# Performance work log

Hardware: AMD Instinct MI355X
Metric: run time of the kernel (lower is better)

## Reference

```python
import jax, jax.numpy as jnp
import numpy as np

N = 30000   # nodes
E = 300000  # edges
B = 64      # graphs
H = 4       # heads
C = 64      # channels per head
HC = H * C  # 256


def setup_inputs() -> dict:
    key = jax.random.key(0)
    ks = jax.random.split(key, 32)

    def rn(k, shape):
        scale = 1.0 / np.sqrt(shape[0])
        return (jax.random.normal(k, shape) * scale).astype(jnp.float32)

    inp = {}
    inp["x"] = jax.random.normal(ks[0], (N, 13), dtype=jnp.float32)
    inp["edge_index"] = jax.random.randint(ks[1], (2, E), 0, N, dtype=jnp.int64)
    inp["edge_attr"] = jax.random.normal(ks[2], (E, 51), dtype=jnp.float32)
    inp["batch"] = jnp.sort(jax.random.randint(ks[3], (N,), 0, B, dtype=jnp.int64))
    # init node MLP: Linear(13 -> 128) (plain_last => no act/norm)
    inp["W0"] = rn(ks[4], (13, 128)); inp["b0"] = jnp.zeros((128,), jnp.float32)
    # GATv2 layer 1: in 128 -> H=4, C=64
    inp["Wl1"] = rn(ks[5], (128, HC)); inp["bl1"] = jnp.zeros((HC,), jnp.float32)
    inp["Wr1"] = rn(ks[6], (128, HC)); inp["br1"] = jnp.zeros((HC,), jnp.float32)
    inp["We1"] = rn(ks[7], (51, HC))
    inp["att1"] = rn(ks[8], (H, C))
    inp["bias1"] = jnp.zeros((HC,), jnp.float32)
    # GATv2 layer 2: in 256 -> H=4, C=64
    inp["Wl2"] = rn(ks[9], (HC, HC)); inp["bl2"] = jnp.zeros((HC,), jnp.float32)
    inp["Wr2"] = rn(ks[10], (HC, HC)); inp["br2"] = jnp.zeros((HC,), jnp.float32)
    inp["We2"] = rn(ks[11], (51, HC))
    inp["att2"] = rn(ks[12], (H, C))
    inp["bias2"] = jnp.zeros((HC,), jnp.float32)
    # attention pooling MLP: Linear(256 -> 256) (plain_last)
    inp["Wp"] = rn(ks[13], (HC, HC)); inp["bp"] = jnp.zeros((HC,), jnp.float32)
    # out MLP: Linear(256->256)+BN+ReLU, Linear(256->2001)
    inp["Wo1"] = rn(ks[14], (HC, 256)); inp["bo1"] = jnp.zeros((256,), jnp.float32)
    inp["gamma"] = jnp.ones((256,), jnp.float32); inp["beta"] = jnp.zeros((256,), jnp.float32)
    inp["Wo2"] = rn(ks[15], (256, 2001)); inp["bo2"] = jnp.zeros((2001,), jnp.float32)
    return inp


def _gatv2(x, src, dst, ea, Wl, bl, Wr, br, We, att, bias):
    n = x.shape[0]
    xl = (x @ Wl + bl).reshape(n, H, C)   # source transform (also message content)
    xr = (x @ Wr + br).reshape(n, H, C)   # target transform
    ee = (ea @ We).reshape(-1, H, C)      # edge embedding, no bias
    z = jax.nn.leaky_relu(xl[src] + xr[dst] + ee, negative_slope=0.2)  # [E,H,C]
    logit = jnp.einsum('ehc,hc->eh', z, att)                           # [E,H]
    m = jax.ops.segment_max(logit, dst, num_segments=n)                # [N,H]
    w = jnp.exp(logit - m[dst])
    den = jax.ops.segment_sum(w, dst, num_segments=n)
    alpha = w / (den[dst] + 1e-16)                                     # segment softmax
    out = jax.ops.segment_sum(xl[src] * alpha[:, :, None], dst, num_segments=n)
    return out.reshape(n, HC) + bias


def _forward(x, edge_index, edge_attr, batch, W0, b0, Wl1, bl1, Wr1, br1, We1, att1, bias1,
             Wl2, bl2, Wr2, br2, We2, att2, bias2, Wp, bp, Wo1, bo1, gamma, beta, Wo2, bo2):
    src, dst = edge_index[0], edge_index[1]
    h = x @ W0 + b0
    h = _gatv2(h, src, dst, edge_attr, Wl1, bl1, Wr1, br1, We1, att1, bias1)
    h = _gatv2(h, src, dst, edge_attr, Wl2, bl2, Wr2, br2, We2, att2, bias2)
    # softmax attention pooling over nodes of each graph (per feature column)
    a = h @ Wp + bp                                       # [N,HC]
    am = jax.ops.segment_max(a, batch, num_segments=B)
    aw = jnp.exp(a - am[batch])
    ad = jax.ops.segment_sum(aw, batch, num_segments=B)
    attw = aw / (ad[batch] + 1e-16)
    g = jax.ops.segment_sum(h * attw, batch, num_segments=B)  # [B,HC]
    # out MLP: Linear + BatchNorm(train stats) + ReLU + Linear, then leaky_relu
    y = g @ Wo1 + bo1
    mu = jnp.mean(y, axis=0)
    var = jnp.var(y, axis=0)
    y = (y - mu) / jnp.sqrt(var + 1e-5) * gamma + beta
    y = jax.nn.relu(y)
    y = y @ Wo2 + bo2
    return jax.nn.leaky_relu(y, negative_slope=0.01)


def reference(x, edge_index, edge_attr, batch, W0, b0, Wl1, bl1, Wr1, br1, We1, att1, bias1,
              Wl2, bl2, Wr2, br2, We2, att2, bias2, Wp, bp, Wo1, bo1, gamma, beta, Wo2, bo2):
    return _forward(x, edge_index, edge_attr, batch, W0, b0, Wl1, bl1, Wr1, br1, We1, att1, bias1,
                    Wl2, bl2, Wr2, br2, We2, att2, bias2, Wp, bp, Wo1, bo1, gamma, beta, Wo2, bo2)
```

## Files before the change

kernel.cpp:

```cpp
#include <hip/hip_runtime.h>
#include <hip/hip_bf16.h>

#define NN 30000
#define EE 300000
#define BB 64
#define HH 4
#define CC 64
#define HC 256

typedef __attribute__((ext_vector_type(8))) short short8;
typedef __attribute__((ext_vector_type(4))) float floatx4;

__device__ __forceinline__ float b2f(short x) {
    return __uint_as_float(((unsigned)(unsigned short)x) << 16);
}
__device__ __forceinline__ unsigned short f2b(float f) {
    __hip_bfloat16 h = __float2bfloat16(f);
    return *(unsigned short*)&h;
}

#define GLD16(gp, lp) __builtin_amdgcn_global_load_lds( \
    (const __attribute__((address_space(1))) void*)(gp), \
    (__attribute__((address_space(3))) void*)(lp), 16, 0, 0)

#define ROT2(x) ((((x) << 2) | ((x) >> 3)) & 31)
#define EESWZ(chunk, row) (ROT2(chunk) ^ (((row) >> 2) & 3) ^ (((row) & 1) << 2))

template<int CT>
__global__ __launch_bounds__(256) void mfma_gemm(
    const ushort* __restrict__ A, const ushort* __restrict__ Bt,
    const float* __restrict__ bias, float* __restrict__ outF,
    __hip_bfloat16* __restrict__ outB, int M, int Nc, int K) {
    __shared__ __align__(16) ushort lA[64 * 32];
    __shared__ __align__(16) ushort lB[CT * 64 * 32];
    const int tid = threadIdx.x, lane = tid & 63, wv = tid >> 6;
    const int row0 = blockIdx.x * 64, col0 = blockIdx.y * (CT * 64);

    floatx4 acc[4][CT];
#pragma unroll
    for (int r = 0; r < 4; r++)
#pragma unroll
        for (int c = 0; c < CT; c++) acc[r][c] = (floatx4){0.f, 0.f, 0.f, 0.f};

    const int arow = tid >> 2;
    const int sl   = (tid & 3) ^ ((tid >> 3) & 3);
    const ushort* ga = A + (size_t)(row0 + arow) * K + sl * 8;
    const int m16 = lane & 15, q = lane >> 4;

    for (int k0 = 0; k0 < K; k0 += 32) {
        __syncthreads();
        GLD16(ga + k0, &lA[tid * 8]);
#pragma unroll
        for (int j = 0; j < CT; j++) {
            const ushort* gb = Bt + (size_t)(col0 + j * 64 + arow) * K + k0 + sl * 8;
            GLD16(gb, &lB[j * 2048 + tid * 8]);
        }
        __syncthreads();
        short8 aF[4], bF[CT];
#pragma unroll
        for (int r = 0; r < 4; r++) {
            int rr = r * 16 + m16;
            aF[r] = *(const short8*)&lA[rr * 32 + ((q ^ ((rr >> 1) & 3)) << 3)];
        }
#pragma unroll
        for (int c = 0; c < CT; c++) {
            int nr = (wv * CT + c) * 16 + m16;
            bF[c] = *(const short8*)&lB[nr * 32 + ((q ^ ((nr >> 1) & 3)) << 3)];
        }
#pragma unroll
        for (int r = 0; r < 4; r++)
#pragma unroll
            for (int c = 0; c < CT; c++)
                acc[r][c] = __builtin_amdgcn_mfma_f32_16x16x32_bf16(aF[r], bF[c], acc[r][c], 0, 0, 0);
    }

#pragma unroll
    for (int c = 0; c < CT; c++) {
        int col = col0 + (wv * CT + c) * 16 + m16;
        float bv = bias ? bias[col] : 0.f;
#pragma unroll
        for (int r = 0; r < 4; r++)
#pragma unroll
            for (int j = 0; j < 4; j++) {
                int row = row0 + r * 16 + q * 4 + j;
                if (row < M) {
                    float v = acc[r][c][j] + bv;
                    if (outB) outB[(size_t)row * Nc + col] = __float2bfloat16(v);
                    else      outF[(size_t)row * Nc + col] = v;
                }
            }
    }
}

__global__ void permute_ea_frag(const float* __restrict__ ea,
                                const int* __restrict__ eidx,
                                ushort* __restrict__ ea_frag) {
    const int t = threadIdx.x, tile = blockIdx.x;
    const int r  = t >> 6;
    const int ch = (t >> 3) & 7;
    const int m0 = (t * 2) & 15;
    ushort* outp = ea_frag + (size_t)tile * 4096 + t * 16;
#pragma unroll
    for (int half = 0; half < 2; half++) {
        int row = r * 16 + m0 + half;
        int gi = tile * 64 + row;
        int e = (gi < EE) ? eidx[gi] : -1;
        short8 v8;
#pragma unroll
        for (int j = 0; j < 8; j++) {
            int k = ch * 8 + j;
            float v = (e >= 0 && k < 51) ? ea[(size_t)e * 51 + k] : 0.f;
            v8[j] = (short)f2b(v);
        }
        *(short8*)(outp + half * 8) = v8;
    }
}

__global__ void pack_we_frag(const float* __restrict__ WeA,
                             const float* __restrict__ WeB,
                             ushort* __restrict__ WfA, ushort* __restrict__ WfB) {
    const float* We = blockIdx.y ? WeB : WeA;
    ushort* Wf = blockIdx.y ? WfB : WfA;
    int o = blockIdx.x * 256 + threadIdx.x;
    int j = o & 7, m16 = (o >> 3) & 15, ch = (o >> 7) & 7, nt = o >> 10;
    int n = nt * 16 + m16, k = ch * 8 + j;
    float v = (k < 51) ? We[k * 256 + n] : 0.f;
    Wf[o] = f2b(v);
}

__global__ __launch_bounds__(256, 4) void edge_fused(
    const ushort* __restrict__ ea_frag, const ushort* __restrict__ Wfrag,
    const float* __restrict__ att,
    const int* __restrict__ src_csr, const int* __restrict__ dst_csr,
    const ushort* __restrict__ xlr, float* __restrict__ logitp) {
    __shared__ __align__(16) ushort eeS[64 * 256];
    __shared__ float satt[256];
    const int tid = threadIdx.x, lane = tid & 63, wv = tid >> 6;
    const int i0 = blockIdx.x * 64;
    satt[tid] = att[tid];
    const int m16 = lane & 15, q = lane >> 4;

    floatx4 acc[4][4];
#pragma unroll
    for (int r = 0; r < 4; r++)
#pragma unroll
        for (int c = 0; c < 4; c++) acc[r][c] = (floatx4){0.f, 0.f, 0.f, 0.f};

    const ushort* af = ea_frag + (size_t)blockIdx.x * 4096;
#pragma unroll
    for (int k0 = 0; k0 < 2; k0++) {
        short8 aF[4], bF[4];
#pragma unroll
        for (int r = 0; r < 4; r++)
            aF[r] = *(const short8*)&af[((r * 8 + k0 * 4 + q) * 16 + m16) * 8];
#pragma unroll
        for (int c = 0; c < 4; c++)
            bF[c] = *(const short8*)&Wfrag[(((wv * 4 + c) * 8 + k0 * 4 + q) * 16 + m16) * 8];
#pragma unroll
        for (int r = 0; r < 4; r++)
#pragma unroll
            for (int c = 0; c < 4; c++)
                acc[r][c] = __builtin_amdgcn_mfma_f32_16x16x32_bf16(aF[r], bF[c], acc[r][c], 0, 0, 0);
    }

#pragma unroll
    for (int r = 0; r < 4; r++)
#pragma unroll
        for (int cc = 0; cc < 4; cc++)
#pragma unroll
            for (int j = 0; j < 4; j++) {
                int row = r * 16 + q * 4 + j;
                int col = (wv * 4 + cc) * 16 + m16;
                int chunk = col >> 3;
                int P = EESWZ(chunk, row);
                eeS[row * 256 + (P << 3) + (col & 7)] = f2b(acc[r][cc][j]);
            }
    __syncthreads();

    const int el = tid >> 2, h = tid & 3;
    const int i = i0 + el;
    if (i < EE) {
        int src = src_csr[i], dstn = dst_csr[i];
        const ushort* xlp = xlr + (size_t)src * 512 + h * 64;
        const ushort* xrp = xlr + (size_t)dstn * 512 + 256 + h * 64;
        float s = 0.f;
#pragma unroll
        for (int c = 0; c < 8; c++) {
            short8 xlv = *(const short8*)(xlp + c * 8);
            short8 xrv = *(const short8*)(xrp + c * 8);
            int chunk = h * 8 + c;
            int P = EESWZ(chunk, el);
            short8 eev = *(const short8*)&eeS[el * 256 + (P << 3)];
#pragma unroll
            for (int j = 0; j < 8; j++) {
                float v = b2f(xlv[j]) + b2f(xrv[j]) + b2f(eev[j]);
                v = v > 0.f ? v : 0.2f * v;
                s += v * satt[h * 64 + c * 8 + j];
            }
        }
        logitp[(size_t)i * 4 + h] = s;
    }
}

__global__ void pack_x(const float* __restrict__ x, __hip_bfloat16* __restrict__ d,
                       int* __restrict__ deg) {
    int i = blockIdx.x * 256 + threadIdx.x;
    if (i < NN) deg[i] = 0;
    if (i >= NN * 32) return;
    int n = i >> 5, k = i & 31;
    d[i] = __float2bfloat16(k < 13 ? x[n * 13 + k] : 0.f);
}
struct PackJob { const float* W; __hip_bfloat16* dst; int K, Nc, Kpad, rowoff; };
struct PackJobs { PackJob j[6]; };
__global__ void pack_all(PackJobs jobs) {
    PackJob jb = jobs.j[blockIdx.y];
    int tot = jb.Nc * jb.Kpad;
    for (int i = blockIdx.x * 256 + threadIdx.x; i < tot; i += gridDim.x * 256) {
        int n = i / jb.Kpad, k = i - n * jb.Kpad;
        float v = (k < jb.K) ? jb.W[k * jb.Nc + n] : 0.f;
        jb.dst[(size_t)(jb.rowoff + n) * jb.Kpad + k] = __float2bfloat16(v);
    }
}
__global__ void cat2(const float* __restrict__ a, const float* __restrict__ b,
                     float* __restrict__ o) {
    int i = blockIdx.x * 256 + threadIdx.x;
    if (i < 512) o[i] = i < 256 ? a[i] : b[i - 256];
}

__global__ void hist_deg(const int* __restrict__ ei, int* __restrict__ deg) {
    int e = blockIdx.x * 256 + threadIdx.x;
    if (e < EE) atomicAdd(&deg[ei[EE + e]], 1);
}
__global__ void scan1(const int* __restrict__ deg, int* __restrict__ partial,
                      int* __restrict__ bsum) {
    __shared__ int sh[256];
    int t = threadIdx.x, i = blockIdx.x * 256 + t;
    int v = (i < NN) ? deg[i] : 0;
    sh[t] = v; __syncthreads();
    for (int off = 1; off < 256; off <<= 1) {
        int x = (t >= off) ? sh[t - off] : 0;
        __syncthreads();
        sh[t] += x;
        __syncthreads();
    }
    if (i < NN) partial[i] = sh[t] - v;
    if (t == 255) bsum[blockIdx.x] = sh[255];
}
__global__ void scan2(int* __restrict__ bsum, int nb) {
    __shared__ int sh[256];
    int t = threadIdx.x;
    int v = (t < nb) ? bsum[t] : 0;
    sh[t] = v; __syncthreads();
    for (int off = 1; off < 256; off <<= 1) {
        int x = (t >= off) ? sh[t - off] : 0;
        __syncthreads();
        sh[t] += x;
        __syncthreads();
    }
    if (t < nb) bsum[t] = sh[t] - v;
}
__global__ void scan3(const int* __restrict__ partial, const int* __restrict__ bsum,
                      int* __restrict__ start, int* __restrict__ cursor) {
    int i = blockIdx.x * 256 + threadIdx.x;
    if (i < NN) { start[i] = partial[i] + bsum[i >> 8]; cursor[i] = 0; }
    else if (i == NN) start[NN] = EE;
}
__global__ void scatter_e(const int* __restrict__ ei, int* __restrict__ cursor,
                          const int* __restrict__ start, int* __restrict__ eidx,
                          int* __restrict__ src_csr, int* __restrict__ dst_csr) {
    int e = blockIdx.x * 256 + threadIdx.x;
    if (e >= EE) return;
    int s = ei[e];
    int d = ei[EE + e];
    int p = atomicAdd(&cursor[d], 1);
    int pos = start[d] + p;
    eidx[pos] = e;
    src_csr[pos] = s;
    dst_csr[pos] = d;
}

__global__ __launch_bounds__(256) void aggregate_csr(
    const ushort* __restrict__ xlr, const float* __restrict__ logitp,
    const int* __restrict__ src_csr, const int* __restrict__ start,
    const float* __restrict__ bias, ushort* __restrict__ outb) {
    const int lane = threadIdx.x & 63, wv = threadIdx.x >> 6;
    const int dst = blockIdx.x * 4 + wv;
    if (dst >= NN) return;
    const int s0 = start[dst];
    const int deg = start[dst + 1] - s0;
    const int h = lane >> 4;

    float m[4] = {-3.4e38f, -3.4e38f, -3.4e38f, -3.4e38f};
    float lg[4] = {0.f, 0.f, 0.f, 0.f};
    int mysrc = 0;
    if (lane < deg) {
        mysrc = src_csr[s0 + lane];
        float4 l4 = ((const float4*)logitp)[s0 + lane];
        lg[0] = l4.x; lg[1] = l4.y; lg[2] = l4.z; lg[3] = l4.w;
        m[0] = l4.x; m[1] = l4.y; m[2] = l4.z; m[3] = l4.w;
    }
    for (int i = 64 + lane; i < deg; i += 64) {
        float4 l4 = ((const float4*)logitp)[s0 + i];
        m[0] = fmaxf(m[0], l4.x); m[1] = fmaxf(m[1], l4.y);
        m[2] = fmaxf(m[2], l4.z); m[3] = fmaxf(m[3], l4.w);
    }
#pragma unroll
    for (int off = 32; off; off >>= 1)
#pragma unroll
        for (int k = 0; k < 4; k++) m[k] = fmaxf(m[k], __shfl_xor(m[k], off));

    float w[4], d[4];
#pragma unroll
    for (int k = 0; k < 4; k++) {
        w[k] = (lane < deg) ? __expf(lg[k] - m[k]) : 0.f;
        d[k] = w[k];
    }
    for (int i = 64 + lane; i < deg; i += 64) {
        float4 l4 = ((const float4*)logitp)[s0 + i];
        d[0] += __expf(l4.x - m[0]); d[1] += __expf(l4.y - m[1]);
        d[2] += __expf(l4.z - m[2]); d[3] += __expf(l4.w - m[3]);
    }
#pragma unroll
    for (int off = 32; off; off >>= 1)
#pragma unroll
        for (int k = 0; k < 4; k++) d[k] += __shfl_xor(d[k], off);
    const float dh = 1.f / (((h == 0) ? d[0] : (h == 1) ? d[1] : (h == 2) ? d[2] : d[3]) + 1e-16f);
    const float mh = (h == 0) ? m[0] : (h == 1) ? m[1] : (h == 2) ? m[2] : m[3];

    float4 b4 = ((const float4*)bias)[lane];
    float a0 = b4.x, a1 = b4.y, a2 = b4.z, a3 = b4.w;

    const int dcap = deg < 64 ? deg : 64;
    const ushort* xbase = xlr + (size_t)lane * 4;
    int i = 0;
    for (; i + 4 <= dcap; i += 4) {
        int sv[4]; float aw[4];
#pragma unroll
        for (int u = 0; u < 4; u++) {
            sv[u] = __shfl(mysrc, i + u);
            float s0v = __shfl(w[0], i + u), s1v = __shfl(w[1], i + u);
            float s2v = __shfl(w[2], i + u), s3v = __shfl(w[3], i + u);
            aw[u] = ((h == 0) ? s0v : (h == 1) ? s1v : (h == 2) ? s2v : s3v) * dh;
        }
        ushort4 xv[4];
#pragma unroll
        for (int u = 0; u < 4; u++)
            xv[u] = *(const ushort4*)(xbase + (size_t)sv[u] * 512);
#pragma unroll
        for (int u = 0; u < 4; u++) {
            a0 += b2f(xv[u].x) * aw[u]; a1 += b2f(xv[u].y) * aw[u];
            a2 += b2f(xv[u].z) * aw[u]; a3 += b2f(xv[u].w) * aw[u];
        }
    }
    for (; i < dcap; i++) {
        int srcv = __shfl(mysrc, i);
        float s0v = __shfl(w[0], i), s1v = __shfl(w[1], i);
        float s2v = __shfl(w[2], i), s3v = __shfl(w[3], i);
        float aw = ((h == 0) ? s0v : (h == 1) ? s1v : (h == 2) ? s2v : s3v) * dh;
        ushort4 xv = *(const ushort4*)(xbase + (size_t)srcv * 512);
        a0 += b2f(xv.x) * aw; a1 += b2f(xv.y) * aw;
        a2 += b2f(xv.z) * aw; a3 += b2f(xv.w) * aw;
    }
    for (int ii = 64; ii < deg; ii++) {
        int srcv = src_csr[s0 + ii];
        float4 l4 = ((const float4*)logitp)[s0 + ii];
        float lh = (h == 0) ? l4.x : (h == 1) ? l4.y : (h == 2) ? l4.z : l4.w;
        float aw = __expf(lh - mh) * dh;
        ushort4 xv = *(const ushort4*)(xbase + (size_t)srcv * 512);
        a0 += b2f(xv.x) * aw; a1 += b2f(xv.y) * aw;
        a2 += b2f(xv.z) * aw; a3 += b2f(xv.w) * aw;
    }
    ushort4 ov;
    ov.x = f2b(a0); ov.y = f2b(a1); ov.z = f2b(a2); ov.w = f2b(a3);
    *(ushort4*)(outb + (size_t)dst * 256 + lane * 4) = ov;
}

__device__ __forceinline__ unsigned fmap(float f) {
    unsigned u = __float_as_uint(f);
    return (u & 0x80000000u) ? ~u : (u | 0x80000000u);
}
__device__ __forceinline__ float funmap(unsigned u) {
    return (u & 0x80000000u) ? __uint_as_float(u & 0x7FFFFFFFu)
                             : __uint_as_float(~u);
}

__global__ void pool_max(const float* __restrict__ a, const int* __restrict__ batch,
                         unsigned* __restrict__ am, float* __restrict__ den,
                         float* __restrict__ num) {
    const int c = threadIdx.x;
    if (blockIdx.x < BB) {
        den[blockIdx.x * HC + c] = 0.f;
        num[blockIdx.x * HC + c] = 0.f;
    }
    const int n0 = blockIdx.x * 64;
    int curb = batch[n0];
    float m = -3.4e38f;
    const int nend = min(n0 + 64, NN);
    for (int n = n0; n < nend; n++) {
        int b = batch[n];
        float v = a[(size_t)n * HC + c];
        if (b != curb) { atomicMax(&am[curb * HC + c], fmap(m)); curb = b; m = v; }
        else           { m = fmaxf(m, v); }
    }
    atomicMax(&am[curb * HC + c], fmap(m));
}
__global__ void pool_sums(const float* __restrict__ a, const __hip_bfloat16* __restrict__ h2,
                          const int* __restrict__ batch, const unsigned* __restrict__ am,
                          float* __restrict__ den, float* __restrict__ num) {
    const int c = threadIdx.x;
    const int n0 = blockIdx.x * 64;
    int curb = batch[n0];
    float sd = 0.f, sn = 0.f;
    float mcur = funmap(am[curb * HC + c]);
    const int nend = min(n0 + 64, NN);
    for (int n = n0; n < nend; n++) {
        int b = batch[n];
        if (b != curb) {
            atomicAdd(&den[curb * HC + c], sd);
            atomicAdd(&num[curb * HC + c], sn);
            curb = b; sd = 0.f; sn = 0.f; mcur = funmap(am[b * HC + c]);
        }
        float w = __expf(a[(size_t)n * HC + c] - mcur);
        sd += w;
        sn += __bfloat162float(h2[(size_t)n * HC + c]) * w;
    }
    atomicAdd(&den[curb * HC + c], sd);
    atomicAdd(&num[curb * HC + c], sn);
}

__global__ void mlp_lin1(const float* __restrict__ num, const float* __restrict__ den,
                         const float* __restrict__ Wo1, const float* __restrict__ bo1,
                         float* __restrict__ y) {
    __shared__ float gsh[HC];
    const int c = threadIdx.x;
    const int r = blockIdx.x;
    gsh[c] = num[r * HC + c] / (den[r * HC + c] + 1e-16f);
    __syncthreads();
    float acc = bo1[c];
#pragma unroll 4
    for (int k = 0; k < HC; k++) acc = fmaf(gsh[k], Wo1[k * HC + c], acc);
    y[r * HC + c] = acc;
}
__global__ void bn_relu(float* __restrict__ y, const float* __restrict__ gamma,
                        const float* __restrict__ beta) {
    const int c = threadIdx.x;
    float s = 0.f, sq = 0.f;
    for (int r = 0; r < BB; r++) { float v = y[r * HC + c]; s += v; sq += v * v; }
    float mu  = s * (1.f / BB);
    float var = sq * (1.f / BB) - mu * mu;
    float inv = rsqrtf(var + 1e-5f) * gamma[c];
    float bt  = beta[c];
    for (int r = 0; r < BB; r++) {
        float v = (y[r * HC + c] - mu) * inv + bt;
        y[r * HC + c] = v > 0.f ? v : 0.f;
    }
}
__global__ void mlp_lin2(const float* __restrict__ y, const float* __restrict__ Wo2,
                         const float* __restrict__ bo2, float* __restrict__ out) {
    const int j = blockIdx.x * 256 + threadIdx.x;
    const int r = blockIdx.y;
    if (j >= 2001) return;
    float acc = bo2[j];
#pragma unroll 4
    for (int k = 0; k < HC; k++) acc = fmaf(y[r * HC + k], Wo2[k * 2001 + j], acc);
    out[r * 2001 + j] = acc > 0.f ? acc : 0.01f * acc;
}

extern "C" void kernel_launch(void* const* d_in, const int* in_sizes, int n_in,
                              void* d_out, int out_size, void* d_ws, size_t ws_size,
                              hipStream_t stream) {
    const float* x     = (const float*)d_in[0];
    const int*   ei    = (const int*)d_in[1];
    const float* ea    = (const float*)d_in[2];
    const int*   batch = (const int*)d_in[3];
    const float* W0 = (const float*)d_in[4];  const float* b0 = (const float*)d_in[5];
    const float* Wl1 = (const float*)d_in[6]; const float* bl1 = (const float*)d_in[7];
    const float* Wr1 = (const float*)d_in[8]; const float* br1 = (const float*)d_in[9];
    const float* We1 = (const float*)d_in[10]; const float* att1 = (const float*)d_in[11];
    const float* bias1 = (const float*)d_in[12];
    const float* Wl2 = (const float*)d_in[13]; const float* bl2 = (const float*)d_in[14];
    const float* Wr2 = (const float*)d_in[15]; const float* br2 = (const float*)d_in[16];
    const float* We2 = (const float*)d_in[17]; const float* att2 = (const float*)d_in[18];
    const float* bias2 = (const float*)d_in[19];
    const float* Wp = (const float*)d_in[20]; const float* bp = (const float*)d_in[21];
    const float* Wo1 = (const float*)d_in[22]; const float* bo1 = (const float*)d_in[23];
    const float* gamma = (const float*)d_in[24]; const float* beta = (const float*)d_in[25];
    const float* Wo2 = (const float*)d_in[26]; const float* bo2 = (const float*)d_in[27];
    float* out = (float*)d_out;

    char* p = (char*)d_ws;
    auto alloc = [&](size_t bytes) { char* r = p; p += (bytes + 255) & ~(size_t)255; return r; };
    const int MP = 30016;
    const int ET = 4688;
    __hip_bfloat16* xpad  = (__hip_bfloat16*)alloc((size_t)MP * 32 * 2);
    __hip_bfloat16* W0t   = (__hip_bfloat16*)alloc(128 * 32 * 2);
    __hip_bfloat16* W1t   = (__hip_bfloat16*)alloc(512 * 128 * 2);
    __hip_bfloat16* W2t   = (__hip_bfloat16*)alloc(512 * 256 * 2);
    __hip_bfloat16* Wpt   = (__hip_bfloat16*)alloc(256 * 256 * 2);
    ushort* Wef1 = (ushort*)alloc(256 * 64 * 2);
    ushort* Wef2 = (ushort*)alloc(256 * 64 * 2);
    float* bcat1 = (float*)alloc(512 * 4);
    float* bcat2 = (float*)alloc(512 * 4);
    __hip_bfloat16* h0b  = (__hip_bfloat16*)alloc((size_t)MP * 128 * 2);
    __hip_bfloat16* xlrb = (__hip_bfloat16*)alloc((size_t)MP * 512 * 2);
    __hip_bfloat16* h1b  = (__hip_bfloat16*)alloc((size_t)MP * 256 * 2);
    __hip_bfloat16* h2b  = (__hip_bfloat16*)alloc((size_t)MP * 256 * 2);
    ushort* ea_frag = (ushort*)alloc((size_t)ET * 4096 * 2);
    float* abuf = (float*)alloc((size_t)MP * 256 * 4);
    float* logit = (float*)alloc((size_t)EE * 4 * 4);
    int* deg    = (int*)alloc(NN * 4);
    int* cursor = (int*)alloc(NN * 4);
    int* partial= (int*)alloc(NN * 4);
    int* bsum   = (int*)alloc(256 * 4);
    int* start  = (int*)alloc((NN + 4) * 4);
    int* eidx   = (int*)alloc((size_t)EE * 4);
    int* src_csr= (int*)alloc((size_t)EE * 4);
    int* dst_csr= (int*)alloc((size_t)EE * 4);
    unsigned* am = (unsigned*)alloc(BB * HC * 4);
    float* den  = (float*)alloc(BB * HC * 4);
    float* num  = (float*)alloc(BB * HC * 4);
    float* ybuf = (float*)alloc(BB * HC * 4);

    const int NB = (NN + 255) / 256;

    pack_x<<<(NN * 32 + 255) / 256, 256, 0, stream>>>(x, xpad, deg);
    PackJobs pj;
    pj.j[0] = {W0,  W0t, 13, 128, 32, 0};
    pj.j[1] = {Wl1, W1t, 128, 256, 128, 0};
    pj.j[2] = {Wr1, W1t, 128, 256, 128, 256};
    pj.j[3] = {Wl2, W2t, 256, 256, 256, 0};
    pj.j[4] = {Wr2, W2t, 256, 256, 256, 256};
    pj.j[5] = {Wp,  Wpt, 256, 256, 256, 0};
    pack_all<<<dim3(64, 6), 256, 0, stream>>>(pj);
    pack_we_frag<<<dim3(64, 2), 256, 0, stream>>>(We1, We2, Wef1, Wef2);
    cat2<<<2, 256, 0, stream>>>(bl1, br1, bcat1);
    cat2<<<2, 256, 0, stream>>>(bl2, br2, bcat2);

    hist_deg<<<(EE + 255) / 256, 256, 0, stream>>>(ei, deg);
    scan1<<<NB, 256, 0, stream>>>(deg, partial, bsum);
    scan2<<<1, 256, 0, stream>>>(bsum, NB);
    scan3<<<NB + 1, 256, 0, stream>>>(partial, bsum, start, cursor);
    scatter_e<<<(EE + 255) / 256, 256, 0, stream>>>(ei, cursor, start, eidx, src_csr, dst_csr);
    permute_ea_frag<<<ET, 256, 0, stream>>>(ea, eidx, ea_frag);

    mfma_gemm<2><<<dim3(469, 1), 256, 0, stream>>>(
        (const ushort*)xpad, (const ushort*)W0t, b0, nullptr, h0b, NN, 128, 32);

    mfma_gemm<4><<<dim3(469, 2), 256, 0, stream>>>(
        (const ushort*)h0b, (const ushort*)W1t, bcat1, nullptr, xlrb, NN, 512, 128);
    edge_fused<<<ET, 256, 0, stream>>>(ea_frag, Wef1, att1, src_csr, dst_csr,
                                       (const ushort*)xlrb, logit);
    aggregate_csr<<<(NN + 3) / 4, 256, 0, stream>>>(
        (const ushort*)xlrb, logit, src_csr, start, bias1, (ushort*)h1b);

    mfma_gemm<4><<<dim3(469, 2), 256, 0, stream>>>(
        (const ushort*)h1b, (const ushort*)W2t, bcat2, nullptr, xlrb, NN, 512, 256);
    edge_fused<<<ET, 256, 0, stream>>>(ea_frag, Wef2, att2, src_csr, dst_csr,
                                       (const ushort*)xlrb, logit);
    aggregate_csr<<<(NN + 3) / 4, 256, 0, stream>>>(
        (const ushort*)xlrb, logit, src_csr, start, bias2, (ushort*)h2b);

    mfma_gemm<4><<<dim3(469, 1), 256, 0, stream>>>(
        (const ushort*)h2b, (const ushort*)Wpt, bp, abuf, nullptr, NN, 256, 256);
    hipMemsetAsync(am, 0, BB * HC * 4, stream);
    const int poolGrid = (NN + 63) / 64;
    pool_max<<<poolGrid, HC, 0, stream>>>(abuf, batch, am, den, num);
    pool_sums<<<poolGrid, HC, 0, stream>>>(abuf, h2b, batch, am, den, num);

    mlp_lin1<<<BB, HC, 0, stream>>>(num, den, Wo1, bo1, ybuf);
    bn_relu<<<1, HC, 0, stream>>>(ybuf, gamma, beta);
    mlp_lin2<<<dim3(8, BB), 256, 0, stream>>>(ybuf, Wo2, bo2, out);
}
```

Measured before the change: 627.2 us.

## Stage bf16 GEMM output through LDS, skip zero K chunk, remap edge tiles

```diff
diff --git a/kernel.cpp b/kernel.cpp
--- a/kernel.cpp
+++ b/kernel.cpp
@@ -31,8 +31,12 @@
     const ushort* __restrict__ A, const ushort* __restrict__ Bt,
     const float* __restrict__ bias, float* __restrict__ outF,
     __hip_bfloat16* __restrict__ outB, int M, int Nc, int K) {
-    __shared__ __align__(16) ushort lA[64 * 32];
-    __shared__ __align__(16) ushort lB[CT * 64 * 32];
+    constexpr int SMEM_USHORTS =
+        ((64 * 32 + CT * 64 * 32) > (64 * CT * 64)) ? (64 * 32 + CT * 64 * 32)
+                                                    : (64 * CT * 64);
+    __shared__ __align__(16) ushort smem[SMEM_USHORTS];
+    ushort* lA = smem;
+    ushort* lB = smem + 64 * 32;
     const int tid = threadIdx.x, lane = tid & 63, wv = tid >> 6;
     const int row0 = blockIdx.x * 64, col0 = blockIdx.y * (CT * 64);
 
@@ -74,21 +78,47 @@
                 acc[r][c] = __builtin_amdgcn_mfma_f32_16x16x32_bf16(aF[r], bF[c], acc[r][c], 0, 0, 0);
     }
 
-#pragma unroll
-    for (int c = 0; c < CT; c++) {
-        int col = col0 + (wv * CT + c) * 16 + m16;
-        float bv = bias ? bias[col] : 0.f;
-#pragma unroll
-        for (int r = 0; r < 4; r++)
-#pragma unroll
-            for (int j = 0; j < 4; j++) {
-                int row = row0 + r * 16 + q * 4 + j;
-                if (row < M) {
-                    float v = acc[r][c][j] + bv;
-                    if (outB) outB[(size_t)row * Nc + col] = __float2bfloat16(v);
-                    else      outF[(size_t)row * Nc + col] = v;
+    if (outB != nullptr) {
+        __syncthreads();
+#pragma unroll
+        for (int c = 0; c < CT; c++) {
+            int lcol = (wv * CT + c) * 16 + m16;
+            float bv = bias ? bias[col0 + lcol] : 0.f;
+            int ch = lcol >> 3, c7 = lcol & 7;
+#pragma unroll
+            for (int r = 0; r < 4; r++)
+#pragma unroll
+                for (int j = 0; j < 4; j++) {
+                    int row = r * 16 + q * 4 + j;
+                    smem[row * (CT * 64) + ((ch ^ (row & 7)) << 3) + c7] =
+                        f2b(acc[r][c][j] + bv);
                 }
+        }
+        __syncthreads();
+        constexpr int SH = (CT == 4) ? 5 : 4;
+#pragma unroll
+        for (int s = 0; s < CT * 2; s++) {
+            int g = tid + 256 * s;
+            int row = g >> SH, ch = g & (CT * 8 - 1);
+            int grow = row0 + row;
+            if (grow < M) {
+                short8 v = *(const short8*)&smem[row * (CT * 64) + ((ch ^ (row & 7)) << 3)];
+                *(short8*)((ushort*)outB + (size_t)grow * Nc + col0 + ch * 8) = v;
             }
+        }
+    } else {
+#pragma unroll
+        for (int c = 0; c < CT; c++) {
+            int col = col0 + (wv * CT + c) * 16 + m16;
+            float bv = bias ? bias[col] : 0.f;
+#pragma unroll
+            for (int r = 0; r < 4; r++)
+#pragma unroll
+                for (int j = 0; j < 4; j++) {
+                    int row = row0 + r * 16 + q * 4 + j;
+                    if (row < M) outF[(size_t)row * Nc + col] = acc[r][c][j] + bv;
+                }
+        }
     }
 }
 
@@ -98,6 +128,7 @@
     const int t = threadIdx.x, tile = blockIdx.x;
     const int r  = t >> 6;
     const int ch = (t >> 3) & 7;
+    if (ch == 7) return;
     const int m0 = (t * 2) & 15;
     ushort* outp = ea_frag + (size_t)tile * 4096 + t * 16;
 #pragma unroll
@@ -136,7 +167,8 @@
     __shared__ __align__(16) ushort eeS[64 * 256];
     __shared__ float satt[256];
     const int tid = threadIdx.x, lane = tid & 63, wv = tid >> 6;
-    const int i0 = blockIdx.x * 64;
+    const int tile = ((int)blockIdx.x & 7) * 586 + ((int)blockIdx.x >> 3);
+    const int i0 = tile * 64;
     satt[tid] = att[tid];
     const int m16 = lane & 15, q = lane >> 4;
 
@@ -146,16 +178,28 @@
 #pragma unroll
         for (int c = 0; c < 4; c++) acc[r][c] = (floatx4){0.f, 0.f, 0.f, 0.f};
 
-    const ushort* af = ea_frag + (size_t)blockIdx.x * 4096;
+    short8 zz;
+#pragma unroll
+    for (int z = 0; z < 8; z++) zz[z] = 0;
+
+    const ushort* af = ea_frag + (size_t)tile * 4096;
 #pragma unroll
     for (int k0 = 0; k0 < 2; k0++) {
         short8 aF[4], bF[4];
-#pragma unroll
-        for (int r = 0; r < 4; r++)
-            aF[r] = *(const short8*)&af[((r * 8 + k0 * 4 + q) * 16 + m16) * 8];
-#pragma unroll
-        for (int c = 0; c < 4; c++)
-            bF[c] = *(const short8*)&Wfrag[(((wv * 4 + c) * 8 + k0 * 4 + q) * 16 + m16) * 8];
+        const bool live = !(k0 == 1 && q == 3);
+        if (live) {
+#pragma unroll
+            for (int r = 0; r < 4; r++)
+                aF[r] = *(const short8*)&af[((r * 8 + k0 * 4 + q) * 16 + m16) * 8];
+#pragma unroll
+            for (int c = 0; c < 4; c++)
+                bF[c] = *(const short8*)&Wfrag[(((wv * 4 + c) * 8 + k0 * 4 + q) * 16 + m16) * 8];
+        } else {
+#pragma unroll
+            for (int r = 0; r < 4; r++) aF[r] = zz;
+#pragma unroll
+            for (int c = 0; c < 4; c++) bF[c] = zz;
+        }
 #pragma unroll
         for (int r = 0; r < 4; r++)
 #pragma unroll
```

Measured after the change: 598.4 us. 4.6% less time.
